# Kernel optimization log

Measured on AMD Instinct MI355X. Metric: run time of the kernel, lower is better.

Reference implementation:

```python
import jax, jax.numpy as jnp
import numpy as np

NUM_LAYERS = 3
NODE_DIM = 32
TIME_DIM = 32
N_HEAD = 4
N_NODES = 1_000_000
BATCH = 256
MODEL_DIM = NODE_DIM + TIME_DIM  # 64
HEAD_DIM = MODEL_DIM // N_HEAD   # 16


def setup_inputs() -> dict:
    key = jax.random.key(0)
    ks = jax.random.split(key, 20)
    L, D, F = NUM_LAYERS, MODEL_DIM, NODE_DIM
    s = 0.1
    return {
        "src_idx": jax.random.randint(ks[0], (BATCH,), 0, N_NODES),
        "target_idx": jax.random.randint(ks[1], (BATCH,), 0, N_NODES),
        "cut_time": jax.random.uniform(ks[2], (BATCH,), dtype=jnp.float32) * 10000.0,
        "num_neighbors": 20,
        # learned params
        "emb": jax.random.uniform(ks[3], (N_NODES, F), minval=-1.0, maxval=1.0, dtype=jnp.float32),
        "time_freq": (1.0 / 10.0 ** jnp.linspace(0.0, 9.0, TIME_DIM)).astype(jnp.float32),
        "time_phase": jnp.zeros((TIME_DIM,), jnp.float32),
        "Wq": jax.random.normal(ks[4], (L, D, D), jnp.float32) * s,
        "Wk": jax.random.normal(ks[5], (L, D, D), jnp.float32) * s,
        "Wv": jax.random.normal(ks[6], (L, D, D), jnp.float32) * s,
        "Wo": jax.random.normal(ks[7], (L, D, D), jnp.float32) * s,
        "mw1": jax.random.normal(ks[8], (L, D + F, F), jnp.float32) * s,
        "mb1": jnp.zeros((L, F), jnp.float32),
        "mw2": jax.random.normal(ks[9], (L, F, F), jnp.float32) * s,
        "mb2": jnp.zeros((L, F), jnp.float32),
        "aff_w1": jax.random.normal(ks[10], (2 * F, F), jnp.float32) * s,
        "aff_b1": jnp.zeros((F,), jnp.float32),
        "aff_w2": jax.random.normal(ks[11], (F, 1), jnp.float32) * s,
        "aff_b2": jnp.zeros((1,), jnp.float32),
    }


def _time_encode(ts, freq, phase):
    # ts: [...]; output [..., TIME_DIM] harmonic encoding (TGAT TimeEncode)
    return jnp.cos(ts[..., None] * freq + phase)


def _sample_neighbors(nodes, times, num_neighbors):
    # Deterministic stand-in for ngh_finder.get_temporal_neighbor (CPU sampler).
    j = jnp.arange(num_neighbors)
    ngh = (nodes[:, None] * 101 + (j + 1) * 7919) % N_NODES        # [n, K] int
    frac = (j + 1).astype(times.dtype) / (num_neighbors + 1)
    ngh_t = times[:, None] * frac                                  # earlier timestamps
    return ngh, ngh_t


def _attn_layer(l, src_feat, src_t_emb, ngh_feat, ngh_t_emb, mask, p):
    # TGAT-style AttnModel: MHA over [feat||time_emb], then MergeLayer(attn_out, src_feat)
    n, K = ngh_feat.shape[0], ngh_feat.shape[1]
    q_in = jnp.concatenate([src_feat, src_t_emb], axis=-1)            # [n, D]
    k_in = jnp.concatenate([ngh_feat, ngh_t_emb], axis=-1)           # [n, K, D]
    q = (q_in @ p["Wq"][l]).reshape(n, N_HEAD, HEAD_DIM)
    k = (k_in @ p["Wk"][l]).reshape(n, K, N_HEAD, HEAD_DIM)
    v = (k_in @ p["Wv"][l]).reshape(n, K, N_HEAD, HEAD_DIM)
    scores = jnp.einsum("nhd,nkhd->nhk", q, k) / jnp.sqrt(jnp.float32(HEAD_DIM))
    scores = jnp.where(mask[:, None, :], -1e9, scores)
    attn = jax.nn.softmax(scores, axis=-1)
    out = jnp.einsum("nhk,nkhd->nhd", attn, v).reshape(n, MODEL_DIM) @ p["Wo"][l]
    h = jax.nn.relu(jnp.concatenate([out, src_feat], axis=-1) @ p["mw1"][l] + p["mb1"][l])
    return h @ p["mw2"][l] + p["mb2"][l]                              # [n, F]


def _tem_conv(nodes, times, layer, num_neighbors, p):
    feat = p["emb"][nodes]                                            # gather [n, F]
    if layer == 0:
        return feat
    src_conv = _tem_conv(nodes, times, layer - 1, num_neighbors, p)   # [n, F]
    ngh, ngh_t = _sample_neighbors(nodes, times, num_neighbors)       # [n, K]
    delta = times[:, None] - ngh_t                                    # [n, K]
    n = nodes.shape[0]
    ngh_conv = _tem_conv(ngh.reshape(-1), ngh_t.reshape(-1), layer - 1,
                         num_neighbors, p).reshape(n, num_neighbors, NODE_DIM)
    src_t_emb = _time_encode(jnp.zeros_like(times), p["time_freq"], p["time_phase"])  # [n, T]
    ngh_t_emb = _time_encode(delta, p["time_freq"], p["time_phase"])  # [n, K, T]
    mask = ngh == 0
    return _attn_layer(layer - 1, src_conv, src_t_emb, ngh_conv, ngh_t_emb, mask, p)


def reference(src_idx, target_idx, cut_time, num_neighbors, emb, time_freq, time_phase,
              Wq, Wk, Wv, Wo, mw1, mb1, mw2, mb2, aff_w1, aff_b1, aff_w2, aff_b2):
    p = dict(emb=emb, time_freq=time_freq, time_phase=time_phase, Wq=Wq, Wk=Wk, Wv=Wv,
             Wo=Wo, mw1=mw1, mb1=mb1, mw2=mw2, mb2=mb2)
    src_embed = _tem_conv(src_idx, cut_time, NUM_LAYERS, num_neighbors, p)
    tgt_embed = _tem_conv(target_idx, cut_time, NUM_LAYERS, num_neighbors, p)
    h = jax.nn.relu(jnp.concatenate([src_embed, tgt_embed], axis=-1) @ aff_w1 + aff_b1)
    return (h @ aff_w2 + aff_b2).squeeze(-1)                          # [B]
```

## Files before the change

### kernel.cpp

```cpp
#include <hip/hip_runtime.h>
#include <math.h>

#define K 20
#define KP1 21
#define F 32
#define NNODES 1000000

#define NP1 112896
#define NP2 5376
#define NP3 256

#define WBLK 16640
#define OFF_H1 49920
#define OFF_H2 (OFF_H1 + 2 * NP1 * F)
#define OFF_H3 (OFF_H2 + 2 * NP2 * F)

#define LDS_M4   12544
#define LDS_WAVE 13568
#define WV_STRIDE 3296
#define SMEM_FLOATS (LDS_WAVE + 8 * WV_STRIDE)

__device__ __forceinline__ int nhash(int node, int j) {
    return (node * 101 + (j + 1) * 7919) % NNODES;
}

__global__ __launch_bounds__(256) void transform_weights(
    const float* __restrict__ Wq, const float* __restrict__ Wk,
    const float* __restrict__ Wv, const float* __restrict__ Wo,
    const float* __restrict__ mw1, const float* __restrict__ mw2,
    const float* __restrict__ phase, float* __restrict__ ws)
{
    const int l = blockIdx.x, tid = threadIdx.x;
    const float* wq = Wq + l * 4096; const float* wk = Wk + l * 4096;
    const float* wv = Wv + l * 4096; const float* wo = Wo + l * 4096;
    const float* m1 = mw1 + l * 3072; const float* m2 = mw2 + l * 1024;
    float* out = ws + l * WBLK;
    for (int i = tid; i < 8192; i += 256) {
        const int a = i >> 8, e = (i >> 2) & 63, h = i & 3;
        float s = 0.f;
        for (int t = 0; t < 16; ++t) s += wq[a * 64 + h * 16 + t] * wk[e * 64 + h * 16 + t];
        out[i] = s;
    }
    for (int i = tid; i < 256; i += 256) {
        const int e = i >> 2, h = i & 3;
        float s = 0.f;
        for (int a = 0; a < 32; ++a) {
            float acc = 0.f;
            for (int t = 0; t < 16; ++t) acc += wq[(32 + a) * 64 + h * 16 + t] * wk[e * 64 + h * 16 + t];
            s += cosf(phase[a]) * acc;
        }
        out[8192 + i] = s;
    }
    for (int i = tid; i < 4096; i += 256) {
        const int e4 = i >> 8, d = (i >> 2) & 63, c = i & 3;
        out[8448 + i] = wv[(4 * e4 + c) * 64 + d];
    }
    for (int i = tid; i < 3072; i += 256) {
        const int k4 = i >> 7, f = (i >> 2) & 31, c = i & 3;
        const int k = 4 * k4 + c;
        float v;
        if (k < 64) { v = 0.f; for (int g2 = 0; g2 < 64; ++g2) v += wo[k * 64 + g2] * m1[g2 * 32 + f]; }
        else v = m1[k * 32 + f];
        out[12544 + i] = v;
    }
    for (int i = tid; i < 1024; i += 256) {
        const int e4 = i >> 7, d = (i >> 2) & 31, c = i & 3;
        out[15616 + i] = m2[(4 * e4 + c) * 32 + d];
    }
}

template<int LEVEL>
__global__ __launch_bounds__(512, 1) void attn_kernel(
    const int* __restrict__ src_idx, const int* __restrict__ tgt_idx,
    const float* __restrict__ cut_time, const float* __restrict__ emb,
    const float* __restrict__ freq, const float* __restrict__ phase,
    const float* __restrict__ ws_w,
    const float* __restrict__ mb1_, const float* __restrict__ mb2_,
    const float* __restrict__ h_in, float* __restrict__ h_out)
{
    constexpr int NPAIRS = (LEVEL == 1) ? NP1 : (LEVEL == 2 ? NP2 : NP3);
    constexpr int PREVN  = (LEVEL == 2) ? NP1 : NP2;
    constexpr int l = LEVEL - 1;

    extern __shared__ float smem[];

    const int tid  = threadIdx.x;
    const int w    = tid >> 6;
    const int lane = tid & 63;
    const int h    = lane >> 4;
    const int c3   = lane & 7;
    const int rep  = (lane >> 3) & 1;
    const int td   = lane & 31;
    const int half = lane >> 5;

    {
        const float* wsrc = ws_w + l * WBLK;
        for (int i4 = tid; i4 < 3136; i4 += 512)
            *(float4*)&smem[i4 * 4] = *(const float4*)&wsrc[i4 * 4];
        for (int i4 = tid; i4 < 256; i4 += 512)
            *(float4*)&smem[LDS_M4 + i4 * 4] = *(const float4*)&wsrc[15616 + i4 * 4];
    }
    __syncthreads();

    float* sM   = smem;
    float* sC   = smem + 8192;
    float* sWv4 = smem + 8448;
    float* sm4  = smem + LDS_M4;
    float* wb   = smem + LDS_WAVE + w * WV_STRIDE;
    float* kin0 = wb;
    float* kin1 = wb + 1280;
    float* qf0  = wb + 2560;
    float* qf1  = wb + 2592;
    float* qz0  = wb + 2624;
    float* qz1  = wb + 2896;
    float* ob0  = wb + 3168;
    float* ob1  = wb + 3232;

    const float* P4g = ws_w + l * WBLK + 12544;

    const float fr = freq[td], ph = phase[td];
    const float b1v = mb1_[l * 32 + td], b2v = mb2_[l * 32 + td];

    const int gstride = gridDim.x * 8;
    float4 pf00, pf01, pf02, pf10, pf11, pf12;
    int na0, na1; float ta;

    const int prow  = lane >> 3, pc4 = lane & 7;
    const int prow1 = (64 + lane) >> 3, pc41 = (64 + lane) & 7;
    const int idx42 = 128 + lane;
    const int prow2 = idx42 >> 3, pc42 = idx42 & 7;

    auto PRE = [&](int p) {
        int b, s2 = 0, r = 0;
        if (LEVEL == 3)      { b = p; }
        else if (LEVEL == 2) { b = p / KP1; s2 = p % KP1; }
        else                 { int qq = p / KP1; r = p % KP1; b = qq / KP1; s2 = qq % KP1; }
        const float ct = cut_time[b];
        const int root0 = src_idx[b];
        const int root1 = tgt_idx[b];
        if (LEVEL == 3) { ta = ct; }
        else if (LEVEL == 2) { ta = s2 ? ct * ((float)s2 / 21.0f) : ct; }
        else {
            const float t2 = s2 ? ct * ((float)s2 / 21.0f) : ct;
            ta = r ? t2 * ((float)r / 21.0f) : t2;
        }
        int nA0, nA1;
        if (LEVEL == 3) { nA0 = root0; nA1 = root1; }
        else if (LEVEL == 2) {
            nA0 = s2 ? nhash(root0, s2 - 1) : root0;
            nA1 = s2 ? nhash(root1, s2 - 1) : root1;
        } else {
            const int n20 = s2 ? nhash(root0, s2 - 1) : root0;
            const int n21 = s2 ? nhash(root1, s2 - 1) : root1;
            nA0 = r ? nhash(n20, r - 1) : n20;
            nA1 = r ? nhash(n21, r - 1) : n21;
        }
        na0 = nA0; na1 = nA1;
        if (LEVEL == 1) {
            { const int node = prow ? nhash(nA0, prow - 1) : nA0;
              pf00 = *(const float4*)&emb[(size_t)node * F + pc4 * 4]; }
            { const int node = nhash(nA0, prow1 - 1);
              pf01 = *(const float4*)&emb[(size_t)node * F + pc41 * 4]; }
            if (idx42 < 168) {
              const int node = nhash(nA0, prow2 - 1);
              pf02 = *(const float4*)&emb[(size_t)node * F + pc42 * 4]; }
            { const int node = prow ? nhash(nA1, prow - 1) : nA1;
              pf10 = *(const float4*)&emb[(size_t)node * F + pc4 * 4]; }
            { const int node = nhash(nA1, prow1 - 1);
              pf11 = *(const float4*)&emb[(size_t)node * F + pc41 * 4]; }
            if (idx42 < 168) {
              const int node = nhash(nA1, prow2 - 1);
              pf12 = *(const float4*)&emb[(size_t)node * F + pc42 * 4]; }
        } else {
            const float* base0 = h_in + ((size_t)p * KP1) * F;
            const float* base1 = h_in + ((size_t)PREVN + (size_t)p * KP1) * F;
            pf00 = *(const float4*)&base0[lane * 4];
            pf01 = *(const float4*)&base0[(64 + lane) * 4];
            if (idx42 < 168) pf02 = *(const float4*)&base0[idx42 * 4];
            pf10 = *(const float4*)&base1[lane * 4];
            pf11 = *(const float4*)&base1[(64 + lane) * 4];
            if (idx42 < 168) pf12 = *(const float4*)&base1[idx42 * 4];
        }
    };

    int g = blockIdx.x * 8 + w;
    if (g < NPAIRS) PRE(g);

    for (; g < NPAIRS; g += gstride) {
        const int gs = g;
        const int cna0 = na0, cna1 = na1;
        const float cta = ta;

        { if (prow == 0) *(float4*)&qf0[pc4 * 4] = pf00;
          else           *(float4*)&kin0[(prow - 1) * 64 + pc4 * 4] = pf00; }
        *(float4*)&kin0[(prow1 - 1) * 64 + pc41 * 4] = pf01;
        if (idx42 < 168) *(float4*)&kin0[(prow2 - 1) * 64 + pc42 * 4] = pf02;
        { if (prow == 0) *(float4*)&qf1[pc4 * 4] = pf10;
          else           *(float4*)&kin1[(prow - 1) * 64 + pc4 * 4] = pf10; }
        *(float4*)&kin1[(prow1 - 1) * 64 + pc41 * 4] = pf11;
        if (idx42 < 168) *(float4*)&kin1[(prow2 - 1) * 64 + pc42 * 4] = pf12;

        #pragma unroll
        for (int it = 0; it < 10; ++it) {
            const int j = it * 2 + half;
            const float ngh_t = cta * ((float)(j + 1) / 21.0f);
            const float delta = cta - ngh_t;
            const float cv = cosf(delta * fr + ph);
            kin0[j * 64 + 32 + td] = cv;
            kin1[j * 64 + 32 + td] = cv;
        }
        unsigned mb0bits, mb1bits;
        { int m = (cna0 * 101 + 7919) % NNODES; unsigned bits = 0;
          #pragma unroll
          for (int j = 0; j < K; ++j) { if (m == 0) bits |= (1u << j); m += 7919; if (m >= NNODES) m -= NNODES; }
          mb0bits = bits; }
        { int m = (cna1 * 101 + 7919) % NNODES; unsigned bits = 0;
          #pragma unroll
          for (int j = 0; j < K; ++j) { if (m == 0) bits |= (1u << j); m += 7919; if (m >= NNODES) m -= NNODES; }
          mb1bits = bits; }

        if (g + gstride < NPAIRS) PRE(g + gstride);

        float4 acc0 = *(const float4*)&sC[lane * 4];
        float4 acc1 = acc0;
        #pragma unroll
        for (int a4 = 0; a4 < 8; ++a4) {
            const float4 f0 = *(float4*)&qf0[a4 * 4];
            const float4 f1 = *(float4*)&qf1[a4 * 4];
            const float4 m0 = *(const float4*)&sM[(a4 * 4 + 0) * 256 + lane * 4];
            const float4 m1v = *(const float4*)&sM[(a4 * 4 + 1) * 256 + lane * 4];
            const float4 m2v = *(const float4*)&sM[(a4 * 4 + 2) * 256 + lane * 4];
            const float4 m3 = *(const float4*)&sM[(a4 * 4 + 3) * 256 + lane * 4];
            acc0.x += f0.x * m0.x + f0.y * m1v.x + f0.z * m2v.x + f0.w * m3.x;
            acc0.y += f0.x * m0.y + f0.y * m1v.y + f0.z * m2v.y + f0.w * m3.y;
            acc0.z += f0.x * m0.z + f0.y * m1v.z + f0.z * m2v.z + f0.w * m3.z;
            acc0.w += f0.x * m0.w + f0.y * m1v.w + f0.z * m2v.w + f0.w * m3.w;
            acc1.x += f1.x * m0.x + f1.y * m1v.x + f1.z * m2v.x + f1.w * m3.x;
            acc1.y += f1.x * m0.y + f1.y * m1v.y + f1.z * m2v.y + f1.w * m3.y;
            acc1.z += f1.x * m0.z + f1.y * m1v.z + f1.z * m2v.z + f1.w * m3.z;
            acc1.w += f1.x * m0.w + f1.y * m1v.w + f1.z * m2v.w + f1.w * m3.w;
        }
        qz0[0 * 68 + lane] = acc0.x; qz0[1 * 68 + lane] = acc0.y;
        qz0[2 * 68 + lane] = acc0.z; qz0[3 * 68 + lane] = acc0.w;
        qz1[0 * 68 + lane] = acc1.x; qz1[1 * 68 + lane] = acc1.y;
        qz1[2 * 68 + lane] = acc1.z; qz1[3 * 68 + lane] = acc1.w;

        const int ofsA = c3 * 8 + rep * 4;
        const int ofsB = c3 * 8 + 4 - rep * 4;
        const int j0 = rep * 10;
        #pragma unroll
        for (int q = 0; q < 2; ++q) {
            float* kin = q ? kin1 : kin0;
            float* qzb = q ? qz1 : qz0;
            const unsigned mbq = q ? mb1bits : mb0bits;
            const float4 qkA = *(float4*)&qzb[h * 68 + ofsA];
            const float4 qkB = *(float4*)&qzb[h * 68 + ofsB];
            float sc[10];
            #pragma unroll
            for (int t = 0; t < 10; ++t) {
                const float4 kA = *(float4*)&kin[(j0 + t) * 64 + ofsA];
                const float4 kB = *(float4*)&kin[(j0 + t) * 64 + ofsB];
                sc[t] = qkA.x * kA.x + qkA.y * kA.y + qkA.z * kA.z + qkA.w * kA.w
                      + qkB.x * kB.x + qkB.y * kB.y + qkB.z * kB.z + qkB.w * kB.w;
            }
            #pragma unroll
            for (int off = 1; off < 8; off <<= 1) {
                #pragma unroll
                for (int t = 0; t < 10; ++t) sc[t] += __shfl_xor(sc[t], off, 8);
            }
            #pragma unroll
            for (int t = 0; t < 10; ++t) {
                float s = sc[t] * 0.25f;
                if ((mbq >> (j0 + t)) & 1) s = -1e9f;
                sc[t] = s;
            }
            float mx = sc[0];
            #pragma unroll
            for (int t = 1; t < 10; ++t) mx = fmaxf(mx, sc[t]);
            mx = fmaxf(mx, __shfl_xor(mx, 8, 16));
            float sum = 0.f;
            #pragma unroll
            for (int t = 0; t < 10; ++t) { sc[t] = __expf(sc[t] - mx); sum += sc[t]; }
            sum += __shfl_xor(sum, 8, 16);
            const float inv = 1.0f / sum;
            float4 zA = {0, 0, 0, 0}, zB = {0, 0, 0, 0};
            #pragma unroll
            for (int t = 0; t < 10; ++t) {
                const float4 kA = *(float4*)&kin[(j0 + t) * 64 + ofsA];
                const float4 kB = *(float4*)&kin[(j0 + t) * 64 + ofsB];
                zA.x += sc[t] * kA.x; zA.y += sc[t] * kA.y; zA.z += sc[t] * kA.z; zA.w += sc[t] * kA.w;
                zB.x += sc[t] * kB.x; zB.y += sc[t] * kB.y; zB.z += sc[t] * kB.z; zB.w += sc[t] * kB.w;
            }
            float4 fA, fB;
            fA.x = zA.x + __shfl_xor(zB.x, 8, 16); fA.y = zA.y + __shfl_xor(zB.y, 8, 16);
            fA.z = zA.z + __shfl_xor(zB.z, 8, 16); fA.w = zA.w + __shfl_xor(zB.w, 8, 16);
            fB.x = zB.x + __shfl_xor(zA.x, 8, 16); fB.y = zB.y + __shfl_xor(zA.y, 8, 16);
            fB.z = zB.z + __shfl_xor(zA.z, 8, 16); fB.w = zB.w + __shfl_xor(zA.w, 8, 16);
            fA.x *= inv; fA.y *= inv; fA.z *= inv; fA.w *= inv;
            fB.x *= inv; fB.y *= inv; fB.z *= inv; fB.w *= inv;
            if (rep == 0) {
                *(float4*)&qzb[h * 68 + ofsA] = fA;
                *(float4*)&qzb[h * 68 + ofsB] = fB;
            }
        }

        float od0 = 0.f, od1 = 0.f;
        #pragma unroll
        for (int e4 = 0; e4 < 16; ++e4) {
            const float4 wv = *(float4*)&sWv4[e4 * 256 + lane * 4];
            const float4 z0 = *(float4*)&qz0[h * 68 + e4 * 4];
            const float4 z1 = *(float4*)&qz1[h * 68 + e4 * 4];
            od0 += z0.x * wv.x + z0.y * wv.y + z0.z * wv.z + z0.w * wv.w;
            od1 += z1.x * wv.x + z1.y * wv.y + z1.z * wv.z + z1.w * wv.w;
        }
        ob0[lane] = od0;
        ob1[lane] = od1;

        float hv0 = 0.f, hv1 = 0.f;
        #pragma unroll
        for (int e4 = 0; e4 < 12; ++e4) {
            float4 x0, x1;
            if (half == 0) { x0 = *(float4*)&ob0[e4 * 4]; x1 = *(float4*)&ob1[e4 * 4]; }
            else {
                x0 = (e4 < 4) ? *(float4*)&ob0[48 + e4 * 4] : *(float4*)&qf0[(e4 - 4) * 4];
                x1 = (e4 < 4) ? *(float4*)&ob1[48 + e4 * 4] : *(float4*)&qf1[(e4 - 4) * 4];
            }
            const float4 w4 = *(const float4*)&P4g[(half * 12 + e4) * 128 + td * 4];
            hv0 += x0.x * w4.x + x0.y * w4.y + x0.z * w4.z + x0.w * w4.w;
            hv1 += x1.x * w4.x + x1.y * w4.y + x1.z * w4.z + x1.w * w4.w;
        }
        hv0 += __shfl_xor(hv0, 32);
        hv1 += __shfl_xor(hv1, 32);
        hv0 = fmaxf(hv0 + b1v, 0.0f);
        hv1 = fmaxf(hv1 + b1v, 0.0f);
        if (lane < 32) { ob0[td] = hv0; ob1[td] = hv1; }

        float y0 = 0.f, y1 = 0.f;
        #pragma unroll
        for (int e4 = 0; e4 < 4; ++e4) {
            const float4 w4 = *(float4*)&sm4[(half * 4 + e4) * 128 + td * 4];
            const float4 x0 = *(float4*)&ob0[half * 16 + e4 * 4];
            const float4 x1 = *(float4*)&ob1[half * 16 + e4 * 4];
            y0 += x0.x * w4.x + x0.y * w4.y + x0.z * w4.z + x0.w * w4.w;
            y1 += x1.x * w4.x + x1.y * w4.y + x1.z * w4.z + x1.w * w4.w;
        }
        y0 += __shfl_xor(y0, 32);
        y1 += __shfl_xor(y1, 32);
        if (lane < 32) {
            h_out[((size_t)0 * NPAIRS + gs) * F + td] = y0 + b2v;
            h_out[((size_t)1 * NPAIRS + gs) * F + td] = y1 + b2v;
        }
    }
}

__global__ __launch_bounds__(256) void final_kernel(
    const float* __restrict__ h3,
    const float* __restrict__ aw1, const float* __restrict__ ab1,
    const float* __restrict__ aw2, const float* __restrict__ ab2,
    float* __restrict__ out)
{
    const int bidx = threadIdx.x;
    float x[64];
    #pragma unroll
    for (int e = 0; e < 32; ++e) {
        x[e]      = h3[(size_t)bidx * 32 + e];
        x[32 + e] = h3[((size_t)NP3 + bidx) * 32 + e];
    }
    float acc = ab2[0];
    for (int f = 0; f < 32; ++f) {
        float hv = ab1[f];
        #pragma unroll
        for (int e = 0; e < 64; ++e) hv += x[e] * aw1[e * 32 + f];
        acc += fmaxf(hv, 0.0f) * aw2[f];
    }
    out[bidx] = acc;
}

extern "C" void kernel_launch(void* const* d_in, const int* in_sizes, int n_in,
                              void* d_out, int out_size, void* d_ws, size_t ws_size,
                              hipStream_t stream)
{
    const int*   src_idx = (const int*)d_in[0];
    const int*   tgt_idx = (const int*)d_in[1];
    const float* cut     = (const float*)d_in[2];
    const float* emb   = (const float*)d_in[4];
    const float* freq  = (const float*)d_in[5];
    const float* phase = (const float*)d_in[6];
    const float* Wq    = (const float*)d_in[7];
    const float* Wk    = (const float*)d_in[8];
    const float* Wv    = (const float*)d_in[9];
    const float* Wo    = (const float*)d_in[10];
    const float* mw1   = (const float*)d_in[11];
    const float* mb1   = (const float*)d_in[12];
    const float* mw2   = (const float*)d_in[13];
    const float* mb2   = (const float*)d_in[14];
    const float* aw1   = (const float*)d_in[15];
    const float* ab1   = (const float*)d_in[16];
    const float* aw2   = (const float*)d_in[17];
    const float* ab2   = (const float*)d_in[18];

    float* ws = (float*)d_ws;
    float* h1 = ws + OFF_H1;
    float* h2 = ws + OFF_H2;
    float* h3 = ws + OFF_H3;

    const size_t smem_bytes = SMEM_FLOATS * sizeof(float);
    hipFuncSetAttribute((const void*)attn_kernel<1>, hipFuncAttributeMaxDynamicSharedMemorySize, (int)smem_bytes);
    hipFuncSetAttribute((const void*)attn_kernel<2>, hipFuncAttributeMaxDynamicSharedMemorySize, (int)smem_bytes);
    hipFuncSetAttribute((const void*)attn_kernel<3>, hipFuncAttributeMaxDynamicSharedMemorySize, (int)smem_bytes);

    transform_weights<<<dim3(3), dim3(256), 0, stream>>>(Wq, Wk, Wv, Wo, mw1, mw2, phase, ws);
    attn_kernel<1><<<dim3(256), dim3(512), smem_bytes, stream>>>(
        src_idx, tgt_idx, cut, emb, freq, phase, ws, mb1, mb2, (const float*)nullptr, h1);
    attn_kernel<2><<<dim3(256), dim3(512), smem_bytes, stream>>>(
        src_idx, tgt_idx, cut, emb, freq, phase, ws, mb1, mb2, h1, h2);
    attn_kernel<3><<<dim3(32), dim3(512), smem_bytes, stream>>>(
        src_idx, tgt_idx, cut, emb, freq, phase, ws, mb1, mb2, h2, h3);
    final_kernel<<<dim3(1), dim3(256), 0, stream>>>(h3, aw1, ab1, aw2, ab2, (float*)d_out);
}
```

Measured before the change: 645.0 us.

## Share time-encoding buffer across src/tgt, fast cosine, closed-form mask, 10 waves per block

The per-wave LDS tile is split into separate feature buffers for the two roots plus one shared time-encoding buffer, so the cosine row is computed and stored once instead of twice. Shrinking the per-wave footprint lets each block hold 10 waves of 640 threads instead of 8, with launch bounds raised to allow more waves per CU. The cosine uses a range-reduced hardware cos intrinsic instead of library cosf, and the 20-step mask loop becomes a closed-form division test. The fast cosine may lose some accuracy for large arguments, and the launch-bounds change limits registers per thread.

Result: slower. 1.105 ms (+71.3%).

```diff
diff --git a/kernel.cpp b/kernel.cpp
--- a/kernel.cpp
+++ b/kernel.cpp
@@ -17,11 +17,28 @@
 
 #define LDS_M4   12544
 #define LDS_WAVE 13568
-#define WV_STRIDE 3296
-#define SMEM_FLOATS (LDS_WAVE + 8 * WV_STRIDE)
+#define WV_STRIDE 2656
+#define SMEM_FLOATS (LDS_WAVE + 10 * WV_STRIDE)
 
 __device__ __forceinline__ int nhash(int node, int j) {
     return (node * 101 + (j + 1) * 7919) % NNODES;
+}
+
+__device__ __forceinline__ float fast_cosf(float x) {
+    const float inv2pi = 0.15915494309189535f;
+    const float k = rintf(x * inv2pi);
+    float r = fmaf(k, -6.28125f, x);
+    r = fmaf(k, -1.9353071795864769e-3f, r);
+    float rev = __builtin_amdgcn_fractf(r * inv2pi);
+    return __builtin_amdgcn_cosf(rev);
+}
+
+__device__ __forceinline__ unsigned mask_bits(int na) {
+    const int m0 = (na * 101) % NNODES;
+    const unsigned d = (unsigned)(NNODES - m0);
+    const unsigned q = d / 7919u;
+    const unsigned rem = d - q * 7919u;
+    return (rem == 0u && (q - 1u) < 20u) ? (1u << (q - 1u)) : 0u;
 }
 
 __global__ __launch_bounds__(256) void transform_weights(
@@ -70,7 +87,7 @@
 }
 
 template<int LEVEL>
-__global__ __launch_bounds__(512, 1) void attn_kernel(
+__global__ __launch_bounds__(640, 3) void attn_kernel(
     const int* __restrict__ src_idx, const int* __restrict__ tgt_idx,
     const float* __restrict__ cut_time, const float* __restrict__ emb,
     const float* __restrict__ freq, const float* __restrict__ phase,
@@ -95,9 +112,9 @@
 
     {
         const float* wsrc = ws_w + l * WBLK;
-        for (int i4 = tid; i4 < 3136; i4 += 512)
+        for (int i4 = tid; i4 < 3136; i4 += 640)
             *(float4*)&smem[i4 * 4] = *(const float4*)&wsrc[i4 * 4];
-        for (int i4 = tid; i4 < 256; i4 += 512)
+        for (int i4 = tid; i4 < 256; i4 += 640)
             *(float4*)&smem[LDS_M4 + i4 * 4] = *(const float4*)&wsrc[15616 + i4 * 4];
     }
     __syncthreads();
@@ -107,21 +124,29 @@
     float* sWv4 = smem + 8448;
     float* sm4  = smem + LDS_M4;
     float* wb   = smem + LDS_WAVE + w * WV_STRIDE;
-    float* kin0 = wb;
-    float* kin1 = wb + 1280;
-    float* qf0  = wb + 2560;
-    float* qf1  = wb + 2592;
-    float* qz0  = wb + 2624;
-    float* qz1  = wb + 2896;
-    float* ob0  = wb + 3168;
-    float* ob1  = wb + 3232;
+    float* kF0  = wb;
+    float* kF1  = wb + 640;
+    float* kT   = wb + 1280;
+    float* qf0  = wb + 1920;
+    float* qf1  = wb + 1952;
+    float* qz0  = wb + 1984;
+    float* qz1  = wb + 2256;
+    float* ob0  = wb + 2528;
+    float* ob1  = wb + 2592;
 
     const float* P4g = ws_w + l * WBLK + 12544;
 
     const float fr = freq[td], ph = phase[td];
     const float b1v = mb1_[l * 32 + td], b2v = mb2_[l * 32 + td];
 
-    const int gstride = gridDim.x * 8;
+    const int ofsA = c3 * 8 + rep * 4;
+    const int ofsB = c3 * 8 + 4 - rep * 4;
+    const float* bA0 = (c3 < 4) ? (kF0 + ofsA) : (kT + ofsA - 32);
+    const float* bB0 = (c3 < 4) ? (kF0 + ofsB) : (kT + ofsB - 32);
+    const float* bA1 = (c3 < 4) ? (kF1 + ofsA) : (kT + ofsA - 32);
+    const float* bB1 = (c3 < 4) ? (kF1 + ofsB) : (kT + ofsB - 32);
+
+    const int gstride = gridDim.x * 10;
     float4 pf00, pf01, pf02, pf10, pf11, pf12;
     int na0, na1; float ta;
 
@@ -183,7 +208,7 @@
         }
     };
 
-    int g = blockIdx.x * 8 + w;
+    int g = blockIdx.x * 10 + w;
     if (g < NPAIRS) PRE(g);
 
     for (; g < NPAIRS; g += gstride) {
@@ -192,32 +217,23 @@
         const float cta = ta;
 
         { if (prow == 0) *(float4*)&qf0[pc4 * 4] = pf00;
-          else           *(float4*)&kin0[(prow - 1) * 64 + pc4 * 4] = pf00; }
-        *(float4*)&kin0[(prow1 - 1) * 64 + pc41 * 4] = pf01;
-        if (idx42 < 168) *(float4*)&kin0[(prow2 - 1) * 64 + pc42 * 4] = pf02;
+          else           *(float4*)&kF0[(prow - 1) * 32 + pc4 * 4] = pf00; }
+        *(float4*)&kF0[(prow1 - 1) * 32 + pc41 * 4] = pf01;
+        if (idx42 < 168) *(float4*)&kF0[(prow2 - 1) * 32 + pc42 * 4] = pf02;
         { if (prow == 0) *(float4*)&qf1[pc4 * 4] = pf10;
-          else           *(float4*)&kin1[(prow - 1) * 64 + pc4 * 4] = pf10; }
-        *(float4*)&kin1[(prow1 - 1) * 64 + pc41 * 4] = pf11;
-        if (idx42 < 168) *(float4*)&kin1[(prow2 - 1) * 64 + pc42 * 4] = pf12;
+          else           *(float4*)&kF1[(prow - 1) * 32 + pc4 * 4] = pf10; }
+        *(float4*)&kF1[(prow1 - 1) * 32 + pc41 * 4] = pf11;
+        if (idx42 < 168) *(float4*)&kF1[(prow2 - 1) * 32 + pc42 * 4] = pf12;
 
         #pragma unroll
         for (int it = 0; it < 10; ++it) {
             const int j = it * 2 + half;
             const float ngh_t = cta * ((float)(j + 1) / 21.0f);
             const float delta = cta - ngh_t;
-            const float cv = cosf(delta * fr + ph);
-            kin0[j * 64 + 32 + td] = cv;
-            kin1[j * 64 + 32 + td] = cv;
-        }
-        unsigned mb0bits, mb1bits;
-        { int m = (cna0 * 101 + 7919) % NNODES; unsigned bits = 0;
-          #pragma unroll
-          for (int j = 0; j < K; ++j) { if (m == 0) bits |= (1u << j); m += 7919; if (m >= NNODES) m -= NNODES; }
-          mb0bits = bits; }
-        { int m = (cna1 * 101 + 7919) % NNODES; unsigned bits = 0;
-          #pragma unroll
-          for (int j = 0; j < K; ++j) { if (m == 0) bits |= (1u << j); m += 7919; if (m >= NNODES) m -= NNODES; }
-          mb1bits = bits; }
+            kT[j * 32 + td] = fast_cosf(delta * fr + ph);
+        }
+        const unsigned mb0bits = mask_bits(cna0);
+        const unsigned mb1bits = mask_bits(cna1);
 
         if (g + gstride < NPAIRS) PRE(g + gstride);
 
@@ -245,12 +261,11 @@
         qz1[0 * 68 + lane] = acc1.x; qz1[1 * 68 + lane] = acc1.y;
         qz1[2 * 68 + lane] = acc1.z; qz1[3 * 68 + lane] = acc1.w;
 
-        const int ofsA = c3 * 8 + rep * 4;
-        const int ofsB = c3 * 8 + 4 - rep * 4;
         const int j0 = rep * 10;
         #pragma unroll
         for (int q = 0; q < 2; ++q) {
-            float* kin = q ? kin1 : kin0;
+            const float* bA = q ? bA1 : bA0;
+            const float* bB = q ? bB1 : bB0;
             float* qzb = q ? qz1 : qz0;
             const unsigned mbq = q ? mb1bits : mb0bits;
             const float4 qkA = *(float4*)&qzb[h * 68 + ofsA];
@@ -258,8 +273,8 @@
             float sc[10];
             #pragma unroll
             for (int t = 0; t < 10; ++t) {
-                const float4 kA = *(float4*)&kin[(j0 + t) * 64 + ofsA];
-                const float4 kB = *(float4*)&kin[(j0 + t) * 64 + ofsB];
+                const float4 kA = *(const float4*)&bA[(j0 + t) * 32];
+                const float4 kB = *(const float4*)&bB[(j0 + t) * 32];
                 sc[t] = qkA.x * kA.x + qkA.y * kA.y + qkA.z * kA.z + qkA.w * kA.w
                       + qkB.x * kB.x + qkB.y * kB.y + qkB.z * kB.z + qkB.w * kB.w;
             }
@@ -286,8 +301,8 @@
             float4 zA = {0, 0, 0, 0}, zB = {0, 0, 0, 0};
             #pragma unroll
             for (int t = 0; t < 10; ++t) {
-                const float4 kA = *(float4*)&kin[(j0 + t) * 64 + ofsA];
-                const float4 kB = *(float4*)&kin[(j0 + t) * 64 + ofsB];
+                const float4 kA = *(const float4*)&bA[(j0 + t) * 32];
+                const float4 kB = *(const float4*)&bB[(j0 + t) * 32];
                 zA.x += sc[t] * kA.x; zA.y += sc[t] * kA.y; zA.z += sc[t] * kA.z; zA.w += sc[t] * kA.w;
                 zB.x += sc[t] * kB.x; zB.y += sc[t] * kB.y; zB.z += sc[t] * kB.z; zB.w += sc[t] * kB.w;
             }
@@ -410,11 +425,11 @@
     hipFuncSetAttribute((const void*)attn_kernel<3>, hipFuncAttributeMaxDynamicSharedMemorySize, (int)smem_bytes);
 
     transform_weights<<<dim3(3), dim3(256), 0, stream>>>(Wq, Wk, Wv, Wo, mw1, mw2, phase, ws);
-    attn_kernel<1><<<dim3(256), dim3(512), smem_bytes, stream>>>(
+    attn_kernel<1><<<dim3(256), dim3(640), smem_bytes, stream>>>(
         src_idx, tgt_idx, cut, emb, freq, phase, ws, mb1, mb2, (const float*)nullptr, h1);
-    attn_kernel<2><<<dim3(256), dim3(512), smem_bytes, stream>>>(
+    attn_kernel<2><<<dim3(256), dim3(640), smem_bytes, stream>>>(
         src_idx, tgt_idx, cut, emb, freq, phase, ws, mb1, mb2, h1, h2);
-    attn_kernel<3><<<dim3(32), dim3(512), smem_bytes, stream>>>(
+    attn_kernel<3><<<dim3(26), dim3(640), smem_bytes, stream>>>(
         src_idx, tgt_idx, cut, emb, freq, phase, ws, mb1, mb2, h2, h3);
     final_kernel<<<dim3(1), dim3(256), 0, stream>>>(h3, aw1, ab1, aw2, ab2, (float*)d_out);
 }
```
